# Performance work log

Hardware: AMD Instinct MI355X
Metric: run time of the kernel (lower is better)

Reference implementation:

```python
import jax, jax.numpy as jnp
import numpy as np

B = 65536  # batch of independent scalar inputs
NQ = 6     # qubits -> state shape (B, 2,2,2,2,2,2); qubit 0 = leftmost axis


def _sel(q, bit, controls):
    ix = [slice(None)] * (NQ + 1)
    for cq in controls:
        ix[cq + 1] = 1
    ix[q + 1] = bit
    return tuple(ix)


def _ry(state, q, theta, controls=()):
    """(Controlled-)RY on qubit q. theta: scalar or (B,) array."""
    half = jnp.asarray(theta) * 0.5
    c, s = jnp.cos(half), jnp.sin(half)
    i0, i1 = _sel(q, 0, controls), _sel(q, 1, controls)
    a0, a1 = state[i0], state[i1]
    if c.ndim:  # batched angle -> broadcast over remaining qubit axes
        bs = (c.shape[0],) + (1,) * (a0.ndim - 1)
        c, s = c.reshape(bs), s.reshape(bs)
    state = state.at[i0].set(c * a0 - s * a1)
    return state.at[i1].set(s * a0 + c * a1)


def _y(state, q, controls=()):
    """(Controlled-)Pauli-Y on qubit q: |0>->i|1>, |1>->-i|0>."""
    i0, i1 = _sel(q, 0, controls), _sel(q, 1, controls)
    a0, a1 = state[i0], state[i1]
    state = state.at[i0].set(-1j * a1)
    return state.at[i1].set(1j * a0)


def _circuit(x, p):
    n = x.shape[0]
    st = jnp.zeros((n,) + (2,) * NQ, jnp.complex64)
    st = st.at[(slice(None),) + (0,) * NQ].set(1.0)
    # -- data encoding block 1 --
    st = _ry(st, 0, x * 3.0); st = _ry(st, 1, x * 9.0); st = _ry(st, 2, x)
    # -- variational layer on qubits 0..2 --
    st = _ry(st, 0, p[0]); st = _ry(st, 1, p[1]); st = _ry(st, 2, p[2])
    # -- controlled rotations onto qubits 3,4,5 --
    st = _ry(st, 3, p[3], (2,)); st = _ry(st, 3, p[4], (1,)); st = _ry(st, 3, p[5], (0,)); st = _ry(st, 3, p[6])
    st = _ry(st, 4, p[7], (2,)); st = _ry(st, 4, p[8], (1,)); st = _ry(st, 4, p[9], (0,)); st = _ry(st, 4, p[10])
    st = _ry(st, 5, p[11], (2,)); st = _ry(st, 5, p[12], (1,)); st = _ry(st, 5, p[13], (0,)); st = _ry(st, 5, p[14])
    st = _ry(st, 3, 0.5); st = _ry(st, 4, 0.5); st = _ry(st, 5, 0.5)
    # -- entangling block among qubits 3,4,5 --
    st = _ry(st, 4, p[15], (3,)); st = _ry(st, 5, p[16], (3,))
    st = _ry(st, 3, p[17], (4,)); st = _ry(st, 5, p[18], (4,))
    st = _ry(st, 3, p[19], (5,)); st = _ry(st, 4, p[20], (5,))
    st = _ry(st, 3, p[21]); st = _ry(st, 4, p[22]); st = _ry(st, 5, p[23])
    # -- triply-controlled Y back onto qubits 0..2 --
    st = _y(st, 0, (3, 4, 5)); st = _y(st, 1, (3, 4, 5)); st = _y(st, 2, (3, 4, 5))
    # -- data encoding block 2 --
    st = _ry(st, 0, x * 7.0); st = _ry(st, 1, x * 17.0); st = _ry(st, 2, x)
    st = _ry(st, 0, p[24]); st = _ry(st, 1, p[25]); st = _ry(st, 2, p[26])
    st = _ry(st, 0, -0.5); st = _ry(st, 1, -0.5); st = _ry(st, 2, -0.5)
    # -- entangling block among qubits 0,1,2 --
    st = _ry(st, 1, p[27], (0,)); st = _ry(st, 2, p[28], (0,))
    st = _ry(st, 0, p[29], (1,)); st = _ry(st, 2, p[30], (1,))
    st = _ry(st, 0, p[31], (2,)); st = _ry(st, 1, p[32], (2,))
    st = _ry(st, 0, p[33]); st = _ry(st, 1, p[34]); st = _ry(st, 2, p[35])
    # marginal probabilities of qubits (0,1,2) being 000 / 111
    p000 = jnp.sum(jnp.abs(st[:, 0, 0, 0]) ** 2, axis=(1, 2, 3))
    p111 = jnp.sum(jnp.abs(st[:, 1, 1, 1]) ** 2, axis=(1, 2, 3))
    return (p111 - p000) * 2.0


def setup_inputs() -> dict:
    key = jax.random.key(0)
    k1, k2 = jax.random.split(key)
    inputs = jax.random.uniform(k1, (B,), dtype=jnp.float32)
    params = jax.random.uniform(k2, (36,), dtype=jnp.float32) * (2.0 * np.pi)
    return {"inputs": inputs, "params": params}


def reference(inputs, params):
    return _circuit(inputs, params)
```

## Files before the change

### kernel.cpp

```cpp
#include <hip/hip_runtime.h>


template <int XM>
__device__ __forceinline__ float lane_perm(float v) {
    int i = __float_as_int(v);
    int r;
    if constexpr (XM == 1)
        r = __builtin_amdgcn_update_dpp(i, i, 0xB1, 0xF, 0xF, 0);
    else if constexpr (XM == 2)
        r = __builtin_amdgcn_update_dpp(i, i, 0x4E, 0xF, 0xF, 0);
    else if constexpr (XM == 4)
        r = __builtin_amdgcn_ds_swizzle(i, 0x101F);
    else
        r = __builtin_amdgcn_update_dpp(i, i, 0x141, 0xF, 0xF, 0);
    return __int_as_float(r);
}

template <int TB, int CB>
__device__ __forceinline__ void ry_r(float* st, float c, float s) {
#pragma unroll
    for (int r = 0; r < 8; ++r) {
        if (r & TB) continue;
        if (CB && !(r & CB)) continue;
        float a0 = st[r], a1 = st[r + TB];
        st[r]      = fmaf(c, a0, -(s * a1));
        st[r + TB] = fmaf(s, a0, c * a1);
    }
}

template <int XM, int LCM>
__device__ __forceinline__ void gate_x(float* st, int lane, float c, float s) {
    float ssgn = (lane & XM) ? s : -s;
    if (LCM) {
        bool act = (lane & LCM) == LCM;
        c = act ? c : 1.0f;
        ssgn = act ? ssgn : 0.0f;
    }
#pragma unroll
    for (int r = 0; r < 8; ++r) {
        float t = c * st[r];
        st[r] = fmaf(ssgn, lane_perm<XM>(st[r]), t);
    }
}

__global__ __launch_bounds__(256) void pnn_kernel(const float* __restrict__ x,
                                                  const float* __restrict__ p,
                                                  float* __restrict__ out,
                                                  int n) {
    __shared__ float2 cs_tab[42];
    {
        int t = threadIdx.x;
        if (t < 42) {
            float th;
            if (t < 24) {
                int tgt = t >> 3, ln = t & 7;
                int base = 3 + 4 * tgt;
                th = p[base + 3] + 0.5f;
                if (ln & 1) th += p[base];
                if (ln & 2) th += p[base + 1];
                if (ln & 4) th += p[base + 2];
            } else if (t < 33) {
                th = p[t - 9];
            } else {
                th = p[t - 6];
            }
            float h = th * 0.5f;
            cs_tab[t] = make_float2(__cosf(h), __sinf(h));
        }
    }
    __syncthreads();

    int gtid = blockIdx.x * blockDim.x + threadIdx.x;
    int e = gtid >> 3;
    int lane = gtid & 7;
    bool live = (e < n);
    int ee = live ? e : 0;
    float xv = x[ee];

    float2 g3 = cs_tab[lane];
    float2 g4 = cs_tab[8 + lane];
    float2 g5 = cs_tab[16 + lane];

    float st[8];
#pragma unroll
    for (int r = 0; r < 8; ++r) st[r] = 0.0f;
    if (lane == 0) st[0] = 1.0f;

    float c, s;
    auto cs = [&](float th) {
        float h = th * 0.5f;
        s = __sinf(h);
        c = __cosf(h);
    };
    auto tab = [&](int k) {
        float2 v = cs_tab[k];
        c = v.x;
        s = v.y;
    };

    cs(fmaf(xv, 3.0f, p[0])); gate_x<4, 0>(st, lane, c, s);
    cs(fmaf(xv, 9.0f, p[1])); gate_x<2, 0>(st, lane, c, s);
    cs(xv + p[2]);            gate_x<1, 0>(st, lane, c, s);

    ry_r<4, 0>(st, g3.x, g3.y);
    ry_r<2, 0>(st, g4.x, g4.y);
    ry_r<1, 0>(st, g5.x, g5.y);

    tab(24); ry_r<2, 4>(st, c, s);
    tab(25); ry_r<1, 4>(st, c, s);
    tab(26); ry_r<4, 2>(st, c, s);
    tab(27); ry_r<1, 2>(st, c, s);
    tab(28); ry_r<4, 1>(st, c, s);
    tab(29); ry_r<2, 1>(st, c, s);
    tab(30); ry_r<4, 0>(st, c, s);
    tab(31); ry_r<2, 0>(st, c, s);
    tab(32); ry_r<1, 0>(st, c, s);

    {
        float ysign = (__popc(lane) & 1) ? -1.0f : 1.0f;
        st[7] = ysign * lane_perm<7>(st[7]);
    }

    cs(fmaf(xv, 7.0f, p[24]) - 0.5f);  gate_x<4, 0>(st, lane, c, s);
    cs(fmaf(xv, 17.0f, p[25]) - 0.5f); gate_x<2, 0>(st, lane, c, s);
    cs(xv + p[26] - 0.5f);             gate_x<1, 0>(st, lane, c, s);

    tab(33); gate_x<2, 4>(st, lane, c, s);
    tab(34); gate_x<1, 4>(st, lane, c, s);
    tab(35); gate_x<4, 2>(st, lane, c, s);
    tab(36); gate_x<1, 2>(st, lane, c, s);
    tab(37); gate_x<4, 1>(st, lane, c, s);
    tab(38); gate_x<2, 1>(st, lane, c, s);
    tab(39); gate_x<4, 0>(st, lane, c, s);
    tab(40); gate_x<2, 0>(st, lane, c, s);
    tab(41); gate_x<1, 0>(st, lane, c, s);

    float psum = 0.0f;
#pragma unroll
    for (int r = 0; r < 8; ++r) psum = fmaf(st[r], st[r], psum);
    float other = lane_perm<7>(psum);
    if (live && lane == 0) out[e] = (other - psum) * 2.0f;
}

extern "C" void kernel_launch(void* const* d_in, const int* in_sizes, int n_in,
                              void* d_out, int out_size, void* d_ws, size_t ws_size,
                              hipStream_t stream) {
    const float* x = (const float*)d_in[0];
    const float* p = (const float*)d_in[1];
    float* out = (float*)d_out;
    int n = in_sizes[0];
    long long threads = (long long)n * 8;
    int block = 256;
    int grid = (int)((threads + block - 1) / block);
    pnn_kernel<<<grid, block, 0, stream>>>(x, p, out, n);
}
```

Baseline: 60.69 us.

## Precompute input-independent circuit blocks as matrices, one thread per sample

Each block now folds the parameter-only middle section of the circuit into an 8x8 real matrix W, and back-propagates the final entangling layer onto the two projectors (000 and 111) as row vectors. These are computed once per block in shared memory. Each thread then handles one sample: it builds a product state from the first encoding rotations, applies the second encoding rotations to the two projector rows, and evaluates the two probabilities with small dense contractions. This replaces the earlier 8-lanes-per-sample state simulation with its cross-lane permutes and cuts the thread count by eight. The trade-off is higher register pressure from holding W in registers, plus an extra block barrier and serial per-block setup work done by a few threads.

```diff
diff --git a/kernel.cpp b/kernel.cpp
--- a/kernel.cpp
+++ b/kernel.cpp
@@ -1,45 +1,26 @@
 #include <hip/hip_runtime.h>
 
 
-template <int XM>
-__device__ __forceinline__ float lane_perm(float v) {
-    int i = __float_as_int(v);
-    int r;
-    if constexpr (XM == 1)
-        r = __builtin_amdgcn_update_dpp(i, i, 0xB1, 0xF, 0xF, 0);
-    else if constexpr (XM == 2)
-        r = __builtin_amdgcn_update_dpp(i, i, 0x4E, 0xF, 0xF, 0);
-    else if constexpr (XM == 4)
-        r = __builtin_amdgcn_ds_swizzle(i, 0x101F);
-    else
-        r = __builtin_amdgcn_update_dpp(i, i, 0x141, 0xF, 0xF, 0);
-    return __int_as_float(r);
-}
-
 template <int TB, int CB>
-__device__ __forceinline__ void ry_r(float* st, float c, float s) {
+__device__ __forceinline__ void ryv(float* m, float c, float s) {
 #pragma unroll
     for (int r = 0; r < 8; ++r) {
         if (r & TB) continue;
         if (CB && !(r & CB)) continue;
-        float a0 = st[r], a1 = st[r + TB];
-        st[r]      = fmaf(c, a0, -(s * a1));
-        st[r + TB] = fmaf(s, a0, c * a1);
+        float a0 = m[r], a1 = m[r + TB];
+        m[r]      = fmaf(c, a0, -(s * a1));
+        m[r + TB] = fmaf(s, a0, c * a1);
     }
 }
 
-template <int XM, int LCM>
-__device__ __forceinline__ void gate_x(float* st, int lane, float c, float s) {
-    float ssgn = (lane & XM) ? s : -s;
-    if (LCM) {
-        bool act = (lane & LCM) == LCM;
-        c = act ? c : 1.0f;
-        ssgn = act ? ssgn : 0.0f;
-    }
+template <int B>
+__device__ __forceinline__ void rmul(float* M, float c, float s) {
 #pragma unroll
-    for (int r = 0; r < 8; ++r) {
-        float t = c * st[r];
-        st[r] = fmaf(ssgn, lane_perm<XM>(st[r]), t);
+    for (int j = 0; j < 8; ++j) {
+        if (j & B) continue;
+        float a = M[j], b = M[j + B];
+        M[j]     = fmaf(c, a, s * b);
+        M[j + B] = fmaf(c, b, -(s * a));
     }
 }
 
@@ -48,98 +29,144 @@
                                                   float* __restrict__ out,
                                                   int n) {
     __shared__ float2 cs_tab[42];
-    {
-        int t = threadIdx.x;
-        if (t < 42) {
-            float th;
-            if (t < 24) {
-                int tgt = t >> 3, ln = t & 7;
-                int base = 3 + 4 * tgt;
-                th = p[base + 3] + 0.5f;
-                if (ln & 1) th += p[base];
-                if (ln & 2) th += p[base + 1];
-                if (ln & 4) th += p[base + 2];
-            } else if (t < 33) {
-                th = p[t - 9];
-            } else {
-                th = p[t - 6];
-            }
-            float h = th * 0.5f;
-            cs_tab[t] = make_float2(__cosf(h), __sinf(h));
+    __shared__ __align__(16) float Wl[8][8];
+    __shared__ __align__(16) float A2r[2][8];
+
+    int t = threadIdx.x;
+    if (t < 42) {
+        float th;
+        if (t < 24) {
+            int tgt = t >> 3, ln = t & 7;
+            int base = 3 + 4 * tgt;
+            th = p[base + 3] + 0.5f;
+            if (ln & 1) th += p[base];
+            if (ln & 2) th += p[base + 1];
+            if (ln & 4) th += p[base + 2];
+        } else if (t < 33) {
+            th = p[t - 9];
+        } else {
+            th = p[t - 6];
         }
+        float h = th * 0.5f;
+        cs_tab[t] = make_float2(__cosf(h), __sinf(h));
     }
     __syncthreads();
 
-    int gtid = blockIdx.x * blockDim.x + threadIdx.x;
-    int e = gtid >> 3;
-    int lane = gtid & 7;
+    int e = blockIdx.x * blockDim.x + t;
     bool live = (e < n);
-    int ee = live ? e : 0;
-    float xv = x[ee];
+    float xv = x[live ? e : 0];
 
-    float2 g3 = cs_tab[lane];
-    float2 g4 = cs_tab[8 + lane];
-    float2 g5 = cs_tab[16 + lane];
+    float h0 = fmaf(1.5f, xv, 0.5f * p[0]);
+    float h1 = fmaf(4.5f, xv, 0.5f * p[1]);
+    float h2 = fmaf(0.5f, xv, 0.5f * p[2]);
+    float h3 = fmaf(3.5f, xv, 0.5f * p[24] - 0.25f);
+    float h4 = fmaf(8.5f, xv, 0.5f * p[25] - 0.25f);
+    float h5 = fmaf(0.5f, xv, 0.5f * p[26] - 0.25f);
+    float c0 = __cosf(h0), s0 = __sinf(h0);
+    float c1 = __cosf(h1), s1 = __sinf(h1);
+    float c2 = __cosf(h2), s2 = __sinf(h2);
+    float gc0 = __cosf(h3), gs0 = __sinf(h3);
+    float gc1 = __cosf(h4), gs1 = __sinf(h4);
+    float gc2 = __cosf(h5), gs2 = __sinf(h5);
 
-    float st[8];
+    float q00 = c1 * c2, q01 = c1 * s2, q10 = s1 * c2, q11 = s1 * s2;
+    float v[8];
+    v[0] = c0 * q00; v[1] = c0 * q01; v[2] = c0 * q10; v[3] = c0 * q11;
+    v[4] = s0 * q00; v[5] = s0 * q01; v[6] = s0 * q10; v[7] = s0 * q11;
+
+    if (t < 8) {
+        float m[8] = {1.f, 0.f, 0.f, 0.f, 0.f, 0.f, 0.f, 0.f};
+        float2 G;
+        G = cs_tab[t];      ryv<4, 0>(m, G.x, G.y);
+        G = cs_tab[8 + t];  ryv<2, 0>(m, G.x, G.y);
+        G = cs_tab[16 + t]; ryv<1, 0>(m, G.x, G.y);
+        G = cs_tab[24]; ryv<2, 4>(m, G.x, G.y);
+        G = cs_tab[25]; ryv<1, 4>(m, G.x, G.y);
+        G = cs_tab[26]; ryv<4, 2>(m, G.x, G.y);
+        G = cs_tab[27]; ryv<1, 2>(m, G.x, G.y);
+        G = cs_tab[28]; ryv<4, 1>(m, G.x, G.y);
+        G = cs_tab[29]; ryv<2, 1>(m, G.x, G.y);
+        G = cs_tab[30]; ryv<4, 0>(m, G.x, G.y);
+        G = cs_tab[31]; ryv<2, 0>(m, G.x, G.y);
+        G = cs_tab[32]; ryv<1, 0>(m, G.x, G.y);
+        float sgn = (__popc(t) & 1) ? -1.f : 1.f;
 #pragma unroll
-    for (int r = 0; r < 8; ++r) st[r] = 0.0f;
-    if (lane == 0) st[0] = 1.0f;
+        for (int r = 0; r < 7; ++r) Wl[t][r] = m[r];
+        Wl[t][7] = sgn * m[7];
+    }
+    if (t == 64 || t == 65) {
+        float w[8] = {0.f, 0.f, 0.f, 0.f, 0.f, 0.f, 0.f, 0.f};
+        w[(t == 64) ? 0 : 7] = 1.f;
+        float2 G;
+        G = cs_tab[41]; ryv<1, 0>(w, G.x, -G.y);
+        G = cs_tab[40]; ryv<2, 0>(w, G.x, -G.y);
+        G = cs_tab[39]; ryv<4, 0>(w, G.x, -G.y);
+        G = cs_tab[38]; ryv<2, 1>(w, G.x, -G.y);
+        G = cs_tab[37]; ryv<4, 1>(w, G.x, -G.y);
+        G = cs_tab[36]; ryv<1, 2>(w, G.x, -G.y);
+        G = cs_tab[35]; ryv<4, 2>(w, G.x, -G.y);
+        G = cs_tab[34]; ryv<1, 4>(w, G.x, -G.y);
+        G = cs_tab[33]; ryv<2, 4>(w, G.x, -G.y);
+#pragma unroll
+        for (int l = 0; l < 8; ++l) A2r[t - 64][l] = w[l];
+    }
+    __syncthreads();
 
-    float c, s;
-    auto cs = [&](float th) {
-        float h = th * 0.5f;
-        s = __sinf(h);
-        c = __cosf(h);
-    };
-    auto tab = [&](int k) {
-        float2 v = cs_tab[k];
-        c = v.x;
-        s = v.y;
-    };
-
-    cs(fmaf(xv, 3.0f, p[0])); gate_x<4, 0>(st, lane, c, s);
-    cs(fmaf(xv, 9.0f, p[1])); gate_x<2, 0>(st, lane, c, s);
-    cs(xv + p[2]);            gate_x<1, 0>(st, lane, c, s);
-
-    ry_r<4, 0>(st, g3.x, g3.y);
-    ry_r<2, 0>(st, g4.x, g4.y);
-    ry_r<1, 0>(st, g5.x, g5.y);
-
-    tab(24); ry_r<2, 4>(st, c, s);
-    tab(25); ry_r<1, 4>(st, c, s);
-    tab(26); ry_r<4, 2>(st, c, s);
-    tab(27); ry_r<1, 2>(st, c, s);
-    tab(28); ry_r<4, 1>(st, c, s);
-    tab(29); ry_r<2, 1>(st, c, s);
-    tab(30); ry_r<4, 0>(st, c, s);
-    tab(31); ry_r<2, 0>(st, c, s);
-    tab(32); ry_r<1, 0>(st, c, s);
-
+    float W[8][8];
+#pragma unroll
+    for (int l = 0; l < 8; ++l) {
+        float4 lo = *(const float4*)&Wl[l][0];
+        float4 hi = *(const float4*)&Wl[l][4];
+        W[l][0] = lo.x; W[l][1] = lo.y; W[l][2] = lo.z; W[l][3] = lo.w;
+        W[l][4] = hi.x; W[l][5] = hi.y; W[l][6] = hi.z; W[l][7] = hi.w;
+    }
+    float M0[8], M1[8];
     {
-        float ysign = (__popc(lane) & 1) ? -1.0f : 1.0f;
-        st[7] = ysign * lane_perm<7>(st[7]);
+        float4 lo = *(const float4*)&A2r[0][0];
+        float4 hi = *(const float4*)&A2r[0][4];
+        M0[0] = lo.x; M0[1] = lo.y; M0[2] = lo.z; M0[3] = lo.w;
+        M0[4] = hi.x; M0[5] = hi.y; M0[6] = hi.z; M0[7] = hi.w;
+        lo = *(const float4*)&A2r[1][0];
+        hi = *(const float4*)&A2r[1][4];
+        M1[0] = lo.x; M1[1] = lo.y; M1[2] = lo.z; M1[3] = lo.w;
+        M1[4] = hi.x; M1[5] = hi.y; M1[6] = hi.z; M1[7] = hi.w;
     }
 
-    cs(fmaf(xv, 7.0f, p[24]) - 0.5f);  gate_x<4, 0>(st, lane, c, s);
-    cs(fmaf(xv, 17.0f, p[25]) - 0.5f); gate_x<2, 0>(st, lane, c, s);
-    cs(xv + p[26] - 0.5f);             gate_x<1, 0>(st, lane, c, s);
+    rmul<4>(M0, gc0, gs0); rmul<4>(M1, gc0, gs0);
+    rmul<2>(M0, gc1, gs1); rmul<2>(M1, gc1, gs1);
+    rmul<1>(M0, gc2, gs2); rmul<1>(M1, gc2, gs2);
 
-    tab(33); gate_x<2, 4>(st, lane, c, s);
-    tab(34); gate_x<1, 4>(st, lane, c, s);
-    tab(35); gate_x<4, 2>(st, lane, c, s);
-    tab(36); gate_x<1, 2>(st, lane, c, s);
-    tab(37); gate_x<4, 1>(st, lane, c, s);
-    tab(38); gate_x<2, 1>(st, lane, c, s);
-    tab(39); gate_x<4, 0>(st, lane, c, s);
-    tab(40); gate_x<2, 0>(st, lane, c, s);
-    tab(41); gate_x<1, 0>(st, lane, c, s);
+    float u0[8], u1[8], z[8];
+#pragma unroll
+    for (int l = 0; l < 8; ++l) {
+        u0[l] = M0[l] * v[l];
+        u1[l] = M1[l] * v[l];
+        z[l]  = W[l ^ 7][7] * v[l ^ 7];
+    }
+    float p000 = 0.f, p111 = 0.f;
+#pragma unroll
+    for (int r = 0; r < 7; ++r) {
+        float a0 = 0.f, a1 = 0.f;
+#pragma unroll
+        for (int l = 0; l < 8; ++l) {
+            a0 = fmaf(u0[l], W[l][r], a0);
+            a1 = fmaf(u1[l], W[l][r], a1);
+        }
+        p000 = fmaf(a0, a0, p000);
+        p111 = fmaf(a1, a1, p111);
+    }
+    {
+        float a0 = 0.f, a1 = 0.f;
+#pragma unroll
+        for (int l = 0; l < 8; ++l) {
+            a0 = fmaf(M0[l], z[l], a0);
+            a1 = fmaf(M1[l], z[l], a1);
+        }
+        p000 = fmaf(a0, a0, p000);
+        p111 = fmaf(a1, a1, p111);
+    }
 
-    float psum = 0.0f;
-#pragma unroll
-    for (int r = 0; r < 8; ++r) psum = fmaf(st[r], st[r], psum);
-    float other = lane_perm<7>(psum);
-    if (live && lane == 0) out[e] = (other - psum) * 2.0f;
+    if (live) out[e] = (p111 - p000) * 2.0f;
 }
 
 extern "C" void kernel_launch(void* const* d_in, const int* in_sizes, int n_in,
@@ -149,8 +176,7 @@
     const float* p = (const float*)d_in[1];
     float* out = (float*)d_out;
     int n = in_sizes[0];
-    long long threads = (long long)n * 8;
     int block = 256;
-    int grid = (int)((threads + block - 1) / block);
+    int grid = (n + block - 1) / block;
     pnn_kernel<<<grid, block, 0, stream>>>(x, p, out, n);
 }
```

Result: faster. 55.77 us (-8.1%).
